# Kernel tuning notes

Measured on AMD Instinct MI355X. Metric: run time of the kernel, lower is better.

## Reference

```python
import jax, jax.numpy as jnp
import numpy as np

N_QUBITS = 8
DEPTH = 2


def _apply1q(state, m00, m01, m10, m11, axis):
    # state: [B, 2, 2, ..., 2]; apply 2x2 gate along `axis`
    s0 = jnp.take(state, 0, axis=axis)
    s1 = jnp.take(state, 1, axis=axis)
    return jnp.stack([m00 * s0 + m01 * s1, m10 * s0 + m11 * s1], axis=axis)


def _cnot(state, ax_c, ax_t):
    # CNOT with control axis ax_c, target axis ax_t = ax_c + 1
    c0 = jnp.take(state, 0, axis=ax_c)
    c1 = jnp.take(state, 1, axis=ax_c)
    c1 = jnp.flip(c1, axis=ax_t - 1)  # target axis shifts left by one after take
    return jnp.stack([c0, c1], axis=ax_c)


def qlayer(angles, rys):
    """Batched state-vector sim of the PennyLane circuit.
    angles: [B, n_qubits] RX encoding angles; rys: [DEPTH, n_qubits].
    Returns <Z_w> per wire: [B, n_qubits] float32.
    (cnot_params in the torch module is unused by the circuit.)"""
    B = angles.shape[0]
    n = N_QUBITS
    state = jnp.zeros((B,) + (2,) * n, jnp.complex64).at[(slice(None),) + (0,) * n].set(1.0)
    bshape = (B,) + (1,) * (n - 1)
    # RX(inputs[q]) on each wire (per-sample angles)
    for q in range(n):
        t = angles[:, q] * 0.5
        c = jnp.cos(t).reshape(bshape).astype(jnp.complex64)
        js = ((-1j) * jnp.sin(t).reshape(bshape)).astype(jnp.complex64)
        state = _apply1q(state, c, js, js, c, q + 1)
    # depth x (RY layer + CNOT chain)
    for d in range(DEPTH):
        for q in range(n):
            t = rys[d, q] * 0.5
            c = jnp.cos(t).astype(jnp.complex64)
            s = jnp.sin(t).astype(jnp.complex64)
            state = _apply1q(state, c, -s, s, c, q + 1)
        for q in range(n - 1):
            state = _cnot(state, q + 1, q + 2)
    probs = state.real ** 2 + state.imag ** 2
    zs = []
    for q in range(n):
        p0 = jnp.take(probs, 0, axis=q + 1).reshape(B, -1).sum(-1)
        p1 = jnp.take(probs, 1, axis=q + 1).reshape(B, -1).sum(-1)
        zs.append(p0 - p1)
    return jnp.stack(zs, axis=1)


def setup_inputs() -> dict:
    key = jax.random.key(0)
    ks = jax.random.split(key, 16)
    T, B, D, H, NQ = 512, 256, 256, 256, N_QUBITS
    lin = lambda k, o, i: (jax.random.normal(k, (o, i), jnp.float32) * np.float32(1.0 / np.sqrt(i)))
    return {
        "inputs": jax.random.normal(ks[0], (T, B, D), jnp.float32),
        "Wf": lin(ks[1], NQ, D + H), "bf": jnp.zeros((NQ,), jnp.float32),
        "Wi": lin(ks[2], NQ, D + H), "bi": jnp.zeros((NQ,), jnp.float32),
        "Wg": lin(ks[3], NQ, D + H), "bg": jnp.zeros((NQ,), jnp.float32),
        "Wo": lin(ks[4], NQ, D + H), "bo": jnp.zeros((NQ,), jnp.float32),
        "rys_f": jax.random.normal(ks[5], (DEPTH, NQ), jnp.float32),
        "rys_i": jax.random.normal(ks[6], (DEPTH, NQ), jnp.float32),
        "rys_g": jax.random.normal(ks[7], (DEPTH, NQ), jnp.float32),
        "rys_o": jax.random.normal(ks[8], (DEPTH, NQ), jnp.float32),
        "Wp": lin(ks[9], H, NQ), "bp": jnp.zeros((H,), jnp.float32),
    }


def reference(inputs, Wf, bf, Wi, bi, Wg, bg, Wo, bo, rys_f, rys_i, rys_g, rys_o, Wp, bp):
    T, B, D = inputs.shape
    H = Wp.shape[0]
    h0 = jnp.zeros((B, H), inputs.dtype)
    c0 = jnp.zeros((B, H), inputs.dtype)

    def step(carry, x):
        hx, cx = carry
        comb = jnp.concatenate([x, hx], axis=1)  # [B, D+H]
        f = jax.nn.sigmoid(qlayer(comb @ Wf.T + bf, rys_f)) @ Wp.T + bp
        i = jax.nn.sigmoid(qlayer(comb @ Wi.T + bi, rys_i)) @ Wp.T + bp
        g = jnp.tanh(qlayer(comb @ Wg.T + bg, rys_g)) @ Wp.T + bp
        o = jax.nn.sigmoid(qlayer(comb @ Wo.T + bo, rys_o)) @ Wp.T + bp
        cx = f * cx + i * g
        hx = o * jnp.tanh(cx)
        return (hx, cx), hx

    (hx, cx), outs = jax.lax.scan(step, (h0, c0), inputs)
    return outs, hx, cx
```

## Files before the change

kernel.cpp:

```cpp
#include <hip/hip_runtime.h>

#define T_STEPS 512
#define BATCH   256
#define DIM     256
#define HID     256
#define NQ      8

#define WG_BARRIER_LDS()                                   \
  do {                                                     \
    __builtin_amdgcn_sched_barrier(0);                     \
    asm volatile("s_waitcnt lgkmcnt(0)" ::: "memory");     \
    __builtin_amdgcn_s_barrier();                          \
    __builtin_amdgcn_sched_barrier(0);                     \
  } while (0)

template <int CTRL>
static __device__ __forceinline__ float dpp_add(float x) {
  int i = __float_as_int(x);
  int j = __builtin_amdgcn_update_dpp(i, i, CTRL, 0xF, 0xF, false);
  return x + __int_as_float(j);
}
#if __has_builtin(__builtin_amdgcn_permlane32_swap)
typedef int v2i_t __attribute__((ext_vector_type(2)));
static __device__ __forceinline__ float xor32_sum(float x) {
  int i = __float_as_int(x);
  v2i_t r = __builtin_amdgcn_permlane32_swap(i, i, false, false);
  return __int_as_float(r.x) + __int_as_float(r.y);
}
#else
static __device__ __forceinline__ float xor32_sum(float x) {
  return x + __shfl_xor(x, 32, 64);
}
#endif


__global__ __launch_bounds__(256, 1)
void qlstm_kernel(const float* __restrict__ inputs,
                  const float* __restrict__ Wf_, const float* __restrict__ bf_,
                  const float* __restrict__ Wi_, const float* __restrict__ bi_,
                  const float* __restrict__ Wg_, const float* __restrict__ bg_,
                  const float* __restrict__ Wo_, const float* __restrict__ bo_,
                  const float* __restrict__ ryf, const float* __restrict__ ryi,
                  const float* __restrict__ ryg, const float* __restrict__ ryo,
                  const float* __restrict__ Wp,  const float* __restrict__ bp,
                  float* __restrict__ out)
{
  const int b    = blockIdx.x;
  const int tid  = threadIdx.x;
  const int w    = tid >> 6;
  const int lane = tid & 63;

  __shared__ float h_lds[HID];
  __shared__ float act[4 * NQ];

  const float* Wgt = (w==0) ? Wf_ : (w==1) ? Wi_ : (w==2) ? Wg_ : Wo_;
  const float* bgt = (w==0) ? bf_ : (w==1) ? bi_ : (w==2) ? bg_ : bo_;
  const float* ry  = (w==0) ? ryf : (w==1) ? ryi : (w==2) ? ryg : ryo;

  float Wc[NQ][8];
#pragma unroll
  for (int q = 0; q < NQ; ++q) {
#pragma unroll
    for (int m = 0; m < 4; ++m) {
      Wc[q][m]     = Wgt[q * 512 + 4 * lane + m];
      Wc[q][4 + m] = Wgt[q * 512 + 256 + 4 * lane + m];
    }
  }

  float bias[NQ];
#pragma unroll
  for (int q = 0; q < NQ; ++q) bias[q] = bgt[q];

  float C0[NQ], S0[NQ], C1c[NQ], S1c[NQ];
#pragma unroll
  for (int q = 0; q < NQ; ++q) {
    sincosf(ry[q],      &S0[q],  &C0[q]);
    sincosf(ry[NQ + q], &S1c[q], &C1c[q]);
  }

  float wp[NQ];
#pragma unroll
  for (int q = 0; q < NQ; ++q) wp[q] = Wp[tid * NQ + q];
  const float bpj = bp[tid];

  float c_reg = 0.f, h_reg = 0.f;
  h_lds[tid] = 0.f;
  __syncthreads();

  const float* xbase = inputs + (size_t)b * DIM + 4 * lane;

  float4 px = *(const float4*)(xbase);

  for (int t = 0; t < T_STEPS; ++t) {
    const float4 xv = px;
    const int tn = (t + 1 < T_STEPS) ? t + 1 : t;
    px = *(const float4*)(xbase + (size_t)tn * BATCH * DIM);

    const float4 hv = *(const float4*)(h_lds + 4 * lane);

    float ang[NQ];
#pragma unroll
    for (int q = 0; q < NQ; ++q) {
      float a = xv.x * Wc[q][0] + xv.y * Wc[q][1] + xv.z * Wc[q][2] + xv.w * Wc[q][3];
      a += hv.x * Wc[q][4] + hv.y * Wc[q][5] + hv.z * Wc[q][6] + hv.w * Wc[q][7];
      ang[q] = a;
    }
#pragma unroll
    for (int q = 0; q < NQ; ++q) ang[q] = dpp_add<0xB1>(ang[q]);
#pragma unroll
    for (int q = 0; q < NQ; ++q) ang[q] = dpp_add<0x4E>(ang[q]);
#pragma unroll
    for (int st = 4; st <= 16; st <<= 1) {
#pragma unroll
      for (int q = 0; q < NQ; ++q) ang[q] += __shfl_xor(ang[q], st, 64);
    }
#pragma unroll
    for (int q = 0; q < NQ; ++q) ang[q] = xor32_sum(ang[q]);

    float EZ[NQ], EXv[NQ], EYv[NQ];
#pragma unroll
    for (int q = 0; q < NQ; ++q) {
      float sA, cA;
      __sincosf(ang[q] + bias[q], &sA, &cA);
      EZ[q]  = C0[q] * cA;
      EXv[q] = S0[q] * cA;
      EYv[q] = -sA;
    }

    float z[NQ];
    float F00 = C1c[0] * EZ[0];
    float F01 = C1c[0];
    float F10 = -S1c[0] * EXv[0];
    float H   = S1c[0] * EYv[0];
    z[0] = F00 + EXv[1] * F10;
#pragma unroll
    for (int k = 1; k < NQ; ++k) {
      const float nF00 = C1c[k] * (EZ[k] * F01 + EYv[k] * H);
      const float nF01 = C1c[k] * (F00 + EXv[k] * F10);
      const float nF10 = -S1c[k] * (EXv[k] * F00 + F10);
      const float nH   =  S1c[k] * (EYv[k] * F01 - EZ[k] * H);
      F00 = nF00; F01 = nF01; F10 = nF10; H = nH;
      z[k] = F00 + ((k < 7) ? EXv[k + 1] : 1.f) * F10;
    }

    float zsel;
    {
      const int l0 = lane & 1, l1 = (lane >> 1) & 1, l2 = (lane >> 2) & 1;
      const float a01 = l0 ? z[1] : z[0];
      const float a23 = l0 ? z[3] : z[2];
      const float a45 = l0 ? z[5] : z[4];
      const float a67 = l0 ? z[7] : z[6];
      const float b03 = l1 ? a23 : a01;
      const float b47 = l1 ? a67 : a45;
      zsel = l2 ? b47 : b03;
    }
    float a_act;
    if (w == 2) {
      const float e = __expf(2.f * zsel);
      a_act = 1.f - 2.f / (e + 1.f);
    } else {
      a_act = 1.f / (1.f + __expf(-zsel));
    }
    if (lane < 8) act[w * NQ + lane] = a_act;
    WG_BARRIER_LDS();

    const float4* a4 = (const float4*)act;
    const float4 f0 = a4[0], f1 = a4[1];
    const float4 i0 = a4[2], i1 = a4[3];
    const float4 g0 = a4[4], g1 = a4[5];
    const float4 o0 = a4[6], o1 = a4[7];
    float fj = bpj, ij = bpj, gj = bpj, oj = bpj;
    fj += f0.x*wp[0] + f0.y*wp[1] + f0.z*wp[2] + f0.w*wp[3]
        + f1.x*wp[4] + f1.y*wp[5] + f1.z*wp[6] + f1.w*wp[7];
    ij += i0.x*wp[0] + i0.y*wp[1] + i0.z*wp[2] + i0.w*wp[3]
        + i1.x*wp[4] + i1.y*wp[5] + i1.z*wp[6] + i1.w*wp[7];
    gj += g0.x*wp[0] + g0.y*wp[1] + g0.z*wp[2] + g0.w*wp[3]
        + g1.x*wp[4] + g1.y*wp[5] + g1.z*wp[6] + g1.w*wp[7];
    oj += o0.x*wp[0] + o0.y*wp[1] + o0.z*wp[2] + o0.w*wp[3]
        + o1.x*wp[4] + o1.y*wp[5] + o1.z*wp[6] + o1.w*wp[7];

    c_reg = fj * c_reg + ij * gj;
    c_reg = fminf(fmaxf(c_reg, -3.0e38f), 3.0e38f);
    const float e2c = __expf(2.f * c_reg);
    const float thc = 1.f - 2.f / (e2c + 1.f);
    h_reg = oj * thc;

    out[((size_t)t * BATCH + b) * HID + tid] = h_reg;
    h_lds[tid] = h_reg;
    WG_BARRIER_LDS();
  }

  out[(size_t)T_STEPS * BATCH * HID + (size_t)b * HID + tid] = h_reg;
  out[(size_t)T_STEPS * BATCH * HID + (size_t)BATCH * HID + (size_t)b * HID + tid] = c_reg;
}

extern "C" void kernel_launch(void* const* d_in, const int* in_sizes, int n_in,
                              void* d_out, int out_size, void* d_ws, size_t ws_size,
                              hipStream_t stream)
{
  const float* inputs = (const float*)d_in[0];
  const float* Wf = (const float*)d_in[1];  const float* bf = (const float*)d_in[2];
  const float* Wi = (const float*)d_in[3];  const float* bi = (const float*)d_in[4];
  const float* Wg = (const float*)d_in[5];  const float* bg = (const float*)d_in[6];
  const float* Wo = (const float*)d_in[7];  const float* bo = (const float*)d_in[8];
  const float* ryf = (const float*)d_in[9];
  const float* ryi = (const float*)d_in[10];
  const float* ryg = (const float*)d_in[11];
  const float* ryo = (const float*)d_in[12];
  const float* Wp = (const float*)d_in[13]; const float* bp = (const float*)d_in[14];
  float* out = (float*)d_out;

  qlstm_kernel<<<dim3(BATCH), dim3(256), 0, stream>>>(
      inputs, Wf, bf, Wi, bi, Wg, bg, Wo, bo, ryf, ryi, ryg, ryo, Wp, bp, out);
}
```

Before: 620.4 us.

## Compute hidden state redundantly per wave, drop second barrier, use DPP row reductions

Each wave now computes the full LSTM cell update for the 4 hidden elements matching its lane slice and keeps h in registers. This removes the h_lds round trip and the second workgroup barrier per timestep, and double-buffers the activation LDS array so one barrier per step is enough. The cross-lane reduction is replaced with a DPP row_shr/row_bcast scan plus readlane instead of shfl_xor and permlane. In exchange, the Wp projection and cell math are repeated in all four waves, roughly quadrupling that arithmetic, and output stores are split across waves.

```diff
diff --git a/kernel.cpp b/kernel.cpp
--- a/kernel.cpp
+++ b/kernel.cpp
@@ -5,6 +5,7 @@
 #define DIM     256
 #define HID     256
 #define NQ      8
+
 
 #define WG_BARRIER_LDS()                                   \
   do {                                                     \
@@ -15,24 +16,20 @@
   } while (0)
 
 template <int CTRL>
-static __device__ __forceinline__ float dpp_add(float x) {
-  int i = __float_as_int(x);
-  int j = __builtin_amdgcn_update_dpp(i, i, CTRL, 0xF, 0xF, false);
+static __device__ __forceinline__ float dpp_add0(float x) {
+  int j = __builtin_amdgcn_update_dpp(0, __float_as_int(x), CTRL, 0xF, 0xF, true);
   return x + __int_as_float(j);
 }
-#if __has_builtin(__builtin_amdgcn_permlane32_swap)
-typedef int v2i_t __attribute__((ext_vector_type(2)));
-static __device__ __forceinline__ float xor32_sum(float x) {
-  int i = __float_as_int(x);
-  v2i_t r = __builtin_amdgcn_permlane32_swap(i, i, false, false);
-  return __int_as_float(r.x) + __int_as_float(r.y);
-}
-#else
-static __device__ __forceinline__ float xor32_sum(float x) {
-  return x + __shfl_xor(x, 32, 64);
-}
-#endif
-
+
+static __device__ __forceinline__ float wave_sum_uniform(float x) {
+  x = dpp_add0<0x111>(x);
+  x = dpp_add0<0x112>(x);
+  x = dpp_add0<0x114>(x);
+  x = dpp_add0<0x118>(x);
+  x = dpp_add0<0x142>(x);
+  x = dpp_add0<0x143>(x);
+  return __int_as_float(__builtin_amdgcn_readlane(__float_as_int(x), 63));
+}
 
 __global__ __launch_bounds__(256, 1)
 void qlstm_kernel(const float* __restrict__ inputs,
@@ -50,8 +47,7 @@
   const int w    = tid >> 6;
   const int lane = tid & 63;
 
-  __shared__ float h_lds[HID];
-  __shared__ float act[4 * NQ];
+  __shared__ float act[2][4 * NQ];
 
   const float* Wgt = (w==0) ? Wf_ : (w==1) ? Wi_ : (w==2) ? Wg_ : Wo_;
   const float* bgt = (w==0) ? bf_ : (w==1) ? bi_ : (w==2) ? bg_ : bo_;
@@ -78,50 +74,49 @@
     sincosf(ry[NQ + q], &S1c[q], &C1c[q]);
   }
 
-  float wp[NQ];
-#pragma unroll
-  for (int q = 0; q < NQ; ++q) wp[q] = Wp[tid * NQ + q];
-  const float bpj = bp[tid];
-
-  float c_reg = 0.f, h_reg = 0.f;
-  h_lds[tid] = 0.f;
-  __syncthreads();
-
-  const float* xbase = inputs + (size_t)b * DIM + 4 * lane;
-
-  float4 px = *(const float4*)(xbase);
+  float wpr[4][NQ];
+  float bpv[4];
+#pragma unroll
+  for (int m = 0; m < 4; ++m) {
+    const int e = 4 * lane + m;
+#pragma unroll
+    for (int q = 0; q < NQ; ++q) wpr[m][q] = Wp[e * NQ + q];
+    bpv[m] = bp[e];
+  }
+
+  float hreg[4] = {0.f, 0.f, 0.f, 0.f};
+  float creg[4] = {0.f, 0.f, 0.f, 0.f};
+
+  const float* xp = inputs + (size_t)b * DIM + 4 * lane;
+  float4 px = *(const float4*)xp;
+
+  float* op = out + (size_t)b * HID;
+
+  int p = 0;
 
   for (int t = 0; t < T_STEPS; ++t) {
     const float4 xv = px;
-    const int tn = (t + 1 < T_STEPS) ? t + 1 : t;
-    px = *(const float4*)(xbase + (size_t)tn * BATCH * DIM);
-
-    const float4 hv = *(const float4*)(h_lds + 4 * lane);
+    if (t + 1 < T_STEPS) {
+      xp += BATCH * DIM;
+      px = *(const float4*)xp;
+    }
 
     float ang[NQ];
 #pragma unroll
     for (int q = 0; q < NQ; ++q) {
       float a = xv.x * Wc[q][0] + xv.y * Wc[q][1] + xv.z * Wc[q][2] + xv.w * Wc[q][3];
-      a += hv.x * Wc[q][4] + hv.y * Wc[q][5] + hv.z * Wc[q][6] + hv.w * Wc[q][7];
+      a += hreg[0] * Wc[q][4] + hreg[1] * Wc[q][5]
+         + hreg[2] * Wc[q][6] + hreg[3] * Wc[q][7];
       ang[q] = a;
     }
 #pragma unroll
-    for (int q = 0; q < NQ; ++q) ang[q] = dpp_add<0xB1>(ang[q]);
-#pragma unroll
-    for (int q = 0; q < NQ; ++q) ang[q] = dpp_add<0x4E>(ang[q]);
-#pragma unroll
-    for (int st = 4; st <= 16; st <<= 1) {
-#pragma unroll
-      for (int q = 0; q < NQ; ++q) ang[q] += __shfl_xor(ang[q], st, 64);
-    }
-#pragma unroll
-    for (int q = 0; q < NQ; ++q) ang[q] = xor32_sum(ang[q]);
+    for (int q = 0; q < NQ; ++q) ang[q] = wave_sum_uniform(ang[q]) + bias[q];
 
     float EZ[NQ], EXv[NQ], EYv[NQ];
 #pragma unroll
     for (int q = 0; q < NQ; ++q) {
       float sA, cA;
-      __sincosf(ang[q] + bias[q], &sA, &cA);
+      __sincosf(ang[q], &sA, &cA);
       EZ[q]  = C0[q] * cA;
       EXv[q] = S0[q] * cA;
       EYv[q] = -sA;
@@ -161,37 +156,49 @@
     } else {
       a_act = 1.f / (1.f + __expf(-zsel));
     }
-    if (lane < 8) act[w * NQ + lane] = a_act;
+    if (lane < 8) act[p][w * NQ + lane] = a_act;
     WG_BARRIER_LDS();
 
-    const float4* a4 = (const float4*)act;
-    const float4 f0 = a4[0], f1 = a4[1];
-    const float4 i0 = a4[2], i1 = a4[3];
-    const float4 g0 = a4[4], g1 = a4[5];
-    const float4 o0 = a4[6], o1 = a4[7];
-    float fj = bpj, ij = bpj, gj = bpj, oj = bpj;
-    fj += f0.x*wp[0] + f0.y*wp[1] + f0.z*wp[2] + f0.w*wp[3]
-        + f1.x*wp[4] + f1.y*wp[5] + f1.z*wp[6] + f1.w*wp[7];
-    ij += i0.x*wp[0] + i0.y*wp[1] + i0.z*wp[2] + i0.w*wp[3]
-        + i1.x*wp[4] + i1.y*wp[5] + i1.z*wp[6] + i1.w*wp[7];
-    gj += g0.x*wp[0] + g0.y*wp[1] + g0.z*wp[2] + g0.w*wp[3]
-        + g1.x*wp[4] + g1.y*wp[5] + g1.z*wp[6] + g1.w*wp[7];
-    oj += o0.x*wp[0] + o0.y*wp[1] + o0.z*wp[2] + o0.w*wp[3]
-        + o1.x*wp[4] + o1.y*wp[5] + o1.z*wp[6] + o1.w*wp[7];
-
-    c_reg = fj * c_reg + ij * gj;
-    c_reg = fminf(fmaxf(c_reg, -3.0e38f), 3.0e38f);
-    const float e2c = __expf(2.f * c_reg);
-    const float thc = 1.f - 2.f / (e2c + 1.f);
-    h_reg = oj * thc;
-
-    out[((size_t)t * BATCH + b) * HID + tid] = h_reg;
-    h_lds[tid] = h_reg;
-    WG_BARRIER_LDS();
-  }
-
-  out[(size_t)T_STEPS * BATCH * HID + (size_t)b * HID + tid] = h_reg;
-  out[(size_t)T_STEPS * BATCH * HID + (size_t)BATCH * HID + (size_t)b * HID + tid] = c_reg;
+    const float4* a4 = (const float4*)act[p];
+    const float4 F0 = a4[0], F1 = a4[1];
+    const float4 I0 = a4[2], I1 = a4[3];
+    const float4 G0 = a4[4], G1 = a4[5];
+    const float4 O0 = a4[6], O1 = a4[7];
+
+    float hv[4];
+#pragma unroll
+    for (int m = 0; m < 4; ++m) {
+      const float* wq = wpr[m];
+      float fj = bpv[m] + F0.x*wq[0] + F0.y*wq[1] + F0.z*wq[2] + F0.w*wq[3]
+                        + F1.x*wq[4] + F1.y*wq[5] + F1.z*wq[6] + F1.w*wq[7];
+      float ij = bpv[m] + I0.x*wq[0] + I0.y*wq[1] + I0.z*wq[2] + I0.w*wq[3]
+                        + I1.x*wq[4] + I1.y*wq[5] + I1.z*wq[6] + I1.w*wq[7];
+      float gj = bpv[m] + G0.x*wq[0] + G0.y*wq[1] + G0.z*wq[2] + G0.w*wq[3]
+                        + G1.x*wq[4] + G1.y*wq[5] + G1.z*wq[6] + G1.w*wq[7];
+      float oj = bpv[m] + O0.x*wq[0] + O0.y*wq[1] + O0.z*wq[2] + O0.w*wq[3]
+                        + O1.x*wq[4] + O1.y*wq[5] + O1.z*wq[6] + O1.w*wq[7];
+      float c = fj * creg[m] + ij * gj;
+      c = fminf(fmaxf(c, -3.0e38f), 3.0e38f);
+      creg[m] = c;
+      const float e2c = __expf(2.f * c);
+      const float thc = 1.f - 2.f / (e2c + 1.f);
+      hv[m] = oj * thc;
+      hreg[m] = hv[m];
+    }
+
+    if ((lane >> 4) == w) {
+      *(float4*)(op + 4 * lane) = make_float4(hv[0], hv[1], hv[2], hv[3]);
+    }
+    op += (size_t)BATCH * HID;
+    p ^= 1;
+  }
+
+  if ((lane >> 4) == w) {
+    float* hx = out + (size_t)T_STEPS * BATCH * HID + (size_t)b * HID;
+    float* cx = hx + (size_t)BATCH * HID;
+    *(float4*)(hx + 4 * lane) = make_float4(hreg[0], hreg[1], hreg[2], hreg[3]);
+    *(float4*)(cx + 4 * lane) = make_float4(creg[0], creg[1], creg[2], creg[3]);
+  }
 }
 
 extern "C" void kernel_launch(void* const* d_in, const int* in_sizes, int n_in,
```

After: 666.9 us. 7.5% more time.
